# Optimization experiments

Hardware: AMD Instinct MI355X
Metric: run time of the kernel (lower is better)

## Reference

```python
import jax, jax.numpy as jnp
import numpy as np

T, B, H, W = 4, 8, 480, 640
N = 4_000_000


def setup_inputs() -> dict:
    key = jax.random.key(0)
    k1, k2, k3, k4 = jax.random.split(key, 4)
    # sorted batch ids (events grouped per sample)
    batch = jnp.sort(jax.random.randint(k1, (N,), 0, B)).astype(jnp.int32)
    # x,y normalized to [0,1]; t sorted globally => sorted within each batch
    xy = jax.random.uniform(k2, (N, 2), dtype=jnp.float32)
    t = jnp.sort(jax.random.uniform(k3, (N,), dtype=jnp.float32))
    pos = jnp.concatenate([xy, t[:, None]], axis=1)  # [N,3]
    feat = jax.random.normal(k4, (N, 1), dtype=jnp.float32)  # polarity = feat[:,0] > 0
    return {"pos": pos, "feat": feat, "batch": batch}


def _voxelize(pos, feat, batch):
    n = pos.shape[0]
    bids = jnp.arange(B, dtype=batch.dtype)
    left = jnp.searchsorted(batch, bids, side="left")
    right = jnporig = jnp.searchsorted(batch, bids, side="right")
    first = jnp.clip(left, 0, n - 1)
    last = jnp.clip(right - 1, 0, n - 1)

    t = pos[:, 2]
    cnt = right - left
    # torch: if t[-1] == t[0] (and >=2 events), bump last event's t by 1
    bump = ((cnt >= 2) & (t[last] == t[first])).astype(t.dtype)
    t = t.at[last].add(bump)

    t0b = t[first]                       # per-batch t[0]
    denom = t[last] - t0b                # per-batch t[-1]-t[0]
    denom = jnp.where(denom == 0, 1.0, denom)  # guard degenerate segments
    tn = (T - 1) * (t - t0b[batch]) / denom[batch]  # [N]

    xf = pos[:, 0] * (W - 1)
    yf = pos[:, 1] * (H - 1)
    x0 = xf.astype(jnp.int32)
    y0 = yf.astype(jnp.int32)
    t0 = tn.astype(jnp.int32)
    ch = jnp.where(feat[:, 0] > 0, 0, 1).astype(jnp.int32)  # pos->chan0, neg->chan1

    # 8 trilinear corners: offsets in {0,1}^3, shape [8,1] broadcast vs [N]
    offs = jnp.array([[dx, dy, dt] for dx in (0, 1) for dy in (0, 1) for dt in (0, 1)], dtype=jnp.int32)
    xl = x0[None, :] + offs[:, 0:1]  # [8,N]
    yl = y0[None, :] + offs[:, 1:2]
    tl = t0[None, :] + offs[:, 2:3]

    m = (xl >= 0) & (xl < W) & (yl >= 0) & (yl < H) & (tl >= 0) & (tl < T)
    w = (1 - jnp.abs(xl - xf[None, :])) * (1 - jnp.abs(yl - yf[None, :])) * (1 - jnp.abs(tl - tn[None, :]))

    bb = batch[None, :].astype(jnp.int32)
    idx = (((tl * B + bb) * 2 + ch[None, :]) * H + yl) * W + xl  # flat into [T,B,2,H,W]
    idx = jnp.where(m, idx, 0)
    w = jnp.where(m, w, 0.0)

    out = jnp.zeros(T * B * 2 * H * W, dtype=jnp.float32).at[idx.ravel()].add(w.ravel())
    return out.reshape(T, B, 2, H, W)


def reference(pos, feat, batch) -> jnp.ndarray:
    return _voxelize(pos, feat, batch)
```

## Files before the change

### kernel.cpp

```cpp
#include <hip/hip_runtime.h>

#define TT 4
#define BB 8
#define HH 480
#define WW 640
#define YSTR 4
#define NYB (HH/YSTR)
#define NBINS2 (BB*TT*NYB)
#define CAP2 2048
#define PPB2 1536
#define FTH 512
#define ITER (PPB2/FTH)
#define SBINS 1024
#define STAGECAP 2112
#define RROWS 4
#define NSTRIPE (HH/RROWS)
#define GTH 512
#define SPILL 0x80000000u
#define FXSCALE 524288.0f
#define FXINV (1.0f/524288.0f)

struct BatchParams { float t0b; float denom; int last; int bump; };

__global__ void setup_kernel(const float* __restrict__ pos, const int* __restrict__ batch,
                             int n, BatchParams* __restrict__ bp, int* __restrict__ rights) {
    int b = threadIdx.x;
    if (b >= BB) return;
    int lo = 0, hi = n;
    while (lo < hi) { int mid = (lo + hi) >> 1; if (batch[mid] < b) lo = mid + 1; else hi = mid; }
    int left = lo;
    lo = left; hi = n;
    while (lo < hi) { int mid = (lo + hi) >> 1; if (batch[mid] <= b) lo = mid + 1; else hi = mid; }
    int right = lo;
    int first = min(max(left, 0), n - 1);
    int last  = min(max(right - 1, 0), n - 1);
    int cnt   = right - left;
    float tf = pos[(size_t)first * 3 + 2];
    float tl = pos[(size_t)last  * 3 + 2];
    int bump = (cnt >= 2 && tl == tf) ? 1 : 0;
    float d = (tl + (float)bump) - tf;
    if (d == 0.0f) d = 1.0f;
    bp[b].t0b = tf; bp[b].denom = d; bp[b].last = last; bp[b].bump = bump;
    rights[b] = right;
}

__device__ __forceinline__ int b_of(const int* __restrict__ sr, int i) {
    int b = 0;
    #pragma unroll
    for (int w = 0; w < BB; ++w) b += (i >= sr[w]) ? 1 : 0;
    return b;
}

__global__ __launch_bounds__(FTH) void fill6_kernel(
        const float* __restrict__ pos, const float* __restrict__ feat,
        const BatchParams* __restrict__ bp, const int* __restrict__ rights,
        unsigned int* __restrict__ cursor, uint2* __restrict__ binidx, int n) {
    __shared__ uint2 stage[STAGECAP];
    __shared__ unsigned int addrbuf[STAGECAP];
    __shared__ unsigned int hist[SBINS];
    __shared__ int          dlt[SBINS];
    __shared__ unsigned int wavesum[8];
    __shared__ unsigned int totloc;
    __shared__ BatchParams sbp[BB];
    __shared__ int sr[BB];
    int tid = threadIdx.x;
    if (tid < BB) { sbp[tid] = bp[tid]; sr[tid] = rights[tid]; }
    hist[2 * tid] = 0; hist[2 * tid + 1] = 0;
    __syncthreads();

    int lo = blockIdx.x * PPB2;

    float px[ITER], py[ITER], ptv[ITER], fv[ITER];
    #pragma unroll
    for (int it = 0; it < ITER; ++it) {
        int i = lo + it * FTH + tid;
        if (i < n) {
            px[it]  = pos[(size_t)i * 3 + 0];
            py[it]  = pos[(size_t)i * 3 + 1];
            ptv[it] = pos[(size_t)i * 3 + 2];
            fv[it]  = feat[i];
        }
    }
    {
        int b0 = b_of(sr, lo);
        BatchParams p0 = sbp[b0];
        float t0v = pos[(size_t)lo * 3 + 2];
        if (p0.bump && lo == p0.last) t0v += 1.0f;
        float tn0 = (float)(TT - 1) * (t0v - p0.t0b) / p0.denom;
        int g_lo = b0 * TT + (int)tn0;
        wavesum[0] = (unsigned int)(g_lo * NYB);
    }
    __syncthreads();
    int binbase_lo = (int)wavesum[0];
    __syncthreads();

    unsigned int rx[ITER], ry[ITER], pm[ITER], ph[ITER];
    int keyv[ITER], hkeyv[ITER];
    #pragma unroll
    for (int it = 0; it < ITER; ++it) {
        int i = lo + it * FTH + tid;
        keyv[it] = -1; hkeyv[it] = -1;
        if (i < n) {
            int b = b_of(sr, i);
            BatchParams p = sbp[b];
            float t = ptv[it];
            if (p.bump && i == p.last) t += 1.0f;
            float tn = (float)(TT - 1) * (t - p.t0b) / p.denom;
            float xf = px[it] * (float)(WW - 1);
            float yf = py[it] * (float)(HH - 1);
            int x0 = (int)xf, y0 = (int)yf, t0 = (int)tn;
            float fx = xf - (float)x0;
            float fy = yf - (float)y0;
            float ft = tn - (float)t0;
            unsigned int ch = (fv[it] > 0.0f) ? 0u : 1u;
            unsigned int rin = (unsigned int)(y0 & 3);
            rx[it] = (unsigned int)x0 | (ch << 10) | (rin << 11)
                   | (((unsigned int)(fx * 4095.0f + 0.5f)) << 20);
            ry[it] = ((unsigned int)(fy * 65535.0f + 0.5f))
                   | (((unsigned int)(ft * 65535.0f + 0.5f)) << 16);
            int g = b * TT + t0;
            int key = g * NYB + (y0 >> 2);
            keyv[it] = key;
            int lb = key - binbase_lo;
            pm[it] = ((unsigned)lb < SBINS) ? atomicAdd(&hist[lb], 1u) : SPILL;
            if (rin == 3u && (y0 >> 2) < NYB - 1) {
                hkeyv[it] = key + 1;
                int lbh = lb + 1;
                ph[it] = ((unsigned)lbh < SBINS) ? atomicAdd(&hist[lbh], 1u) : SPILL;
            }
        }
    }
    __syncthreads();
    unsigned int c0 = hist[2 * tid], c1 = hist[2 * tid + 1];
    unsigned int sum = c0 + c1;
    int lane = tid & 63, wid = tid >> 6;
    unsigned int scan = sum;
    #pragma unroll
    for (int off = 1; off < 64; off <<= 1) {
        unsigned int v = __shfl_up(scan, off, 64);
        if (lane >= off) scan += v;
    }
    if (lane == 63) wavesum[wid] = scan;
    __syncthreads();
    unsigned int woff = 0;
    #pragma unroll
    for (int w = 0; w < 8; ++w) woff += (w < wid) ? wavesum[w] : 0u;
    unsigned int incl = woff + scan;
    unsigned int base = incl - sum;
    if (tid == FTH - 1) totloc = incl;
    {
        unsigned int lp0 = base, lp1 = base + c0;
        int bin0 = binbase_lo + 2 * tid;
        unsigned int gb0 = 0, gb1 = 0;
        if (c0 && (unsigned)bin0     < NBINS2) gb0 = atomicAdd(&cursor[bin0],     c0);
        if (c1 && (unsigned)(bin0+1) < NBINS2) gb1 = atomicAdd(&cursor[bin0 + 1], c1);
        dlt[2 * tid]     = (int)gb0 - (int)lp0;
        dlt[2 * tid + 1] = (int)gb1 - (int)lp1;
        hist[2 * tid] = lp0; hist[2 * tid + 1] = lp1;
    }
    __syncthreads();
    #pragma unroll
    for (int it = 0; it < ITER; ++it) {
        if (keyv[it] < 0) continue;
        #pragma unroll
        for (int h = 0; h < 2; ++h) {
            int key = h ? hkeyv[it] : keyv[it];
            if (key < 0) continue;
            unsigned int p = h ? ph[it] : pm[it];
            uint2 rec; rec.x = h ? (rx[it] | (1u << 13)) : rx[it]; rec.y = ry[it];
            if (p & SPILL) {
                unsigned int slot = atomicAdd(&cursor[key], 1u);
                if (slot < CAP2) binidx[(size_t)key * CAP2 + slot] = rec;
            } else {
                int lb = key - binbase_lo;
                unsigned int sl = hist[lb] + p;
                unsigned int off = (unsigned int)(dlt[lb] + (int)sl);
                if (sl < STAGECAP) {
                    stage[sl] = rec;
                    addrbuf[sl] = (off < CAP2) ? (unsigned int)key * CAP2 + off
                                               : 0xFFFFFFFFu;
                } else if (off < CAP2) {
                    binidx[(size_t)key * CAP2 + off] = rec;
                }
            }
        }
    }
    __syncthreads();
    unsigned int tot = min(totloc, (unsigned int)STAGECAP);
    for (unsigned int k = tid; k < tot; k += FTH) {
        unsigned int a = addrbuf[k];
        if (a != 0xFFFFFFFFu) binidx[a] = stage[k];
    }
}

__device__ __forceinline__ void gather_rec(unsigned long long* tile, uint2 rec, int q) {
    int x0   = (int)(rec.x & 1023u);
    int ch   = (int)((rec.x >> 10) & 1u);
    int rin  = (int)((rec.x >> 11) & 3u);
    int halo = (int)((rec.x >> 13) & 1u);
    float fx = (float)((rec.x >> 20) & 4095u) * (1.0f / 4095.0f);
    float fy = (float)(rec.y & 65535u) * (1.0f / 65535.0f);
    float ft = (float)(rec.y >> 16) * (1.0f / 65535.0f);
    float wt = q ? (1.0f - ft) : ft;
    float w1 = wt * fy;
    unsigned long long p1 =
          (unsigned long long)(unsigned int)fmaf(w1 * (1.0f - fx), FXSCALE, 0.5f)
        | ((unsigned long long)(unsigned int)fmaf(w1 * fx, FXSCALE, 0.5f) << 32);
    if (halo) {
        atomicAdd(&tile[(ch * RROWS) * WW + x0], p1);
    } else {
        float w0 = wt * (1.0f - fy);
        unsigned long long p0 =
              (unsigned long long)(unsigned int)fmaf(w0 * (1.0f - fx), FXSCALE, 0.5f)
            | ((unsigned long long)(unsigned int)fmaf(w0 * fx, FXSCALE, 0.5f) << 32);
        unsigned long long* rowp = &tile[(ch * RROWS + rin) * WW + x0];
        atomicAdd(rowp, p0);
        if (rin < RROWS - 1) atomicAdd(rowp + WW, p1);
    }
}

__global__ __launch_bounds__(GTH) void gather7_kernel(
        const unsigned int* __restrict__ cursor, const uint2* __restrict__ binidx,
        float* __restrict__ out) {
    __shared__ unsigned long long tile[2 * RROWS * WW];
    __shared__ unsigned int cnt[2];
    int bid = blockIdx.x;
    int s  = bid % NSTRIPE;
    int bt = bid / NSTRIPE;
    int tl = bt % TT;
    int b  = bt / TT;
    int r0 = s * RROWS;
    int tid = threadIdx.x;

    if (tid < 2) {
        int t0r = tl - 1 + tid;
        unsigned int c = 0;
        if (t0r >= 0) c = min(cursor[(b * TT + t0r) * NYB + s], (unsigned int)CAP2);
        cnt[tid] = c;
    }
    for (int k = tid; k < 2 * RROWS * WW; k += GTH) tile[k] = 0ull;
    __syncthreads();

    #pragma unroll
    for (int q = 0; q < 2; ++q) {
        int t0r = tl - 1 + q;
        if (t0r < 0) continue;
        unsigned int base = (unsigned int)((b * TT + t0r) * NYB + s) * CAP2;
        unsigned int c = cnt[q];
        unsigned int m = tid;
        if (m < c) {
            uint2 rec = binidx[base + m];
            for (;;) {
                unsigned int m2 = m + GTH;
                bool has2 = m2 < c;
                uint2 rec2;
                if (has2) rec2 = binidx[base + m2];
                gather_rec(tile, rec, q);
                if (!has2) break;
                rec = rec2; m = m2;
            }
        }
    }
    __syncthreads();
    const unsigned int* t32 = (const unsigned int*)tile;
    const int QUADS = 2 * RROWS * WW / 4;
    for (int qd = tid; qd < QUADS; qd += GTH) {
        int e = qd * 4;
        uint4 A = *(const uint4*)&t32[e * 2];
        uint4 B = *(const uint4*)&t32[e * 2 + 4];
        unsigned int cc = (e % WW == 0) ? 0u : t32[e * 2 - 1];
        float4 v;
        v.x = (float)(A.x + cc)  * FXINV;
        v.y = (float)(A.z + A.y) * FXINV;
        v.z = (float)(B.x + A.w) * FXINV;
        v.w = (float)(B.z + B.y) * FXINV;
        int ch  = e / (RROWS * WW);
        int rem = e % (RROWS * WW);
        int r   = rem / WW;
        int x   = rem % WW;
        *(float4*)&out[((((size_t)tl * BB + b) * 2 + ch) * HH + (r0 + r)) * WW + x] = v;
    }
}

__global__ void voxel_kernel(const float* __restrict__ pos, const float* __restrict__ feat,
                             const int* __restrict__ batch, const BatchParams* __restrict__ bp,
                             float* __restrict__ out, int n) {
    __shared__ BatchParams sbp[BB];
    if (threadIdx.x < BB) sbp[threadIdx.x] = bp[threadIdx.x];
    __syncthreads();
    int i = blockIdx.x * blockDim.x + threadIdx.x;
    if (i >= n) return;
    int b = batch[i];
    float x = pos[(size_t)i * 3 + 0];
    float y = pos[(size_t)i * 3 + 1];
    float t = pos[(size_t)i * 3 + 2];
    BatchParams p = sbp[b];
    if (p.bump && i == p.last) t += 1.0f;
    float tn = (float)(TT - 1) * (t - p.t0b) / p.denom;
    float xf = x * (float)(WW - 1);
    float yf = y * (float)(HH - 1);
    int x0 = (int)xf, y0 = (int)yf, t0 = (int)tn;
    float fx = xf - (float)x0, fy = yf - (float)y0, ft = tn - (float)t0;
    int ch = (feat[i] > 0.0f) ? 0 : 1;
    float wx[2] = {1.0f - fx, fx};
    float wy[2] = {1.0f - fy, fy};
    float wt[2] = {1.0f - ft, ft};
    #pragma unroll
    for (int dt = 0; dt < 2; ++dt) {
        int tlc = t0 + dt;
        if (tlc < 0 || tlc >= TT) continue;
        #pragma unroll
        for (int dy = 0; dy < 2; ++dy) {
            int yl = y0 + dy;
            if (yl < 0 || yl >= HH) continue;
            #pragma unroll
            for (int dx = 0; dx < 2; ++dx) {
                int xl = x0 + dx;
                if (xl < 0 || xl >= WW) continue;
                float w = wx[dx] * wy[dy] * wt[dt];
                size_t idx = ((((size_t)tlc * BB + b) * 2 + ch) * (size_t)HH + yl) * (size_t)WW + xl;
                atomicAdd(&out[idx], w);
            }
        }
    }
}

extern "C" void kernel_launch(void* const* d_in, const int* in_sizes, int n_in,
                              void* d_out, int out_size, void* d_ws, size_t ws_size,
                              hipStream_t stream) {
    const float* pos   = (const float*)d_in[0];
    const float* feat  = (const float*)d_in[1];
    const int*   batch = (const int*)d_in[2];
    float* out = (float*)d_out;
    int n = in_sizes[2];

    char* ws = (char*)d_ws;
    BatchParams* bp      = (BatchParams*)ws;
    int*          rights = (int*)(ws + 512);
    unsigned int* cursor = (unsigned int*)(ws + 1024);
    uint2*        binidx = (uint2*)(ws + 65536);
    size_t need = 65536 + (size_t)NBINS2 * CAP2 * sizeof(uint2);

    if (ws_size >= need) {
        hipMemsetAsync(cursor, 0, NBINS2 * sizeof(unsigned int), stream);
        setup_kernel<<<1, 64, 0, stream>>>(pos, batch, n, bp, rights);
        int nblocks = (n + PPB2 - 1) / PPB2;
        fill6_kernel<<<nblocks, FTH, 0, stream>>>(pos, feat, bp, rights, cursor, binidx, n);
        gather7_kernel<<<BB * TT * NSTRIPE, GTH, 0, stream>>>(cursor, binidx, out);
    } else {
        hipMemsetAsync(d_out, 0, (size_t)out_size * sizeof(float), stream);
        setup_kernel<<<1, 64, 0, stream>>>(pos, batch, n, bp, rights);
        int blocks = (n + 255) / 256;
        voxel_kernel<<<blocks, 256, 0, stream>>>(pos, feat, batch, bp, out, n);
    }
}
```

Before: 91.93 us.

## Split stripe bins into main and halo sub-bins instead of duplicating halo records

Events whose y falls in the last row of a 4-row stripe are no longer written twice, once to their own bin and once as a halo copy to the next stripe. Each stripe now has two sub-bins: a main bin (cap 1280) and a row-3 bin (cap 512). The gather kernel reads the main bin, its own row-3 bin and the previous stripe's row-3 bin, then applies the matching row weights. This removes the duplicate writes and shrinks both the workspace and the staging buffer. The trade-off is fixed per-bin capacities that could drop events if a sub-bin overflows, and removed staging-overflow guards that assume the staging buffer always fits.

```diff
diff --git a/kernel.cpp b/kernel.cpp
--- a/kernel.cpp
+++ b/kernel.cpp
@@ -6,13 +6,16 @@
 #define WW 640
 #define YSTR 4
 #define NYB (HH/YSTR)
-#define NBINS2 (BB*TT*NYB)
-#define CAP2 2048
+#define NSTRIPES (BB*TT*NYB)
+#define CAPA 1280
+#define CAPB 512
+#define STRCAP (CAPA+CAPB)
+#define NKEYS (NSTRIPES*2)
 #define PPB2 1536
 #define FTH 512
 #define ITER (PPB2/FTH)
 #define SBINS 1024
-#define STAGECAP 2112
+#define STAGECAP 1536
 #define RROWS 4
 #define NSTRIPE (HH/RROWS)
 #define GTH 512
@@ -51,7 +54,7 @@
     return b;
 }
 
-__global__ __launch_bounds__(FTH) void fill6_kernel(
+__global__ __launch_bounds__(FTH) void fill7_kernel(
         const float* __restrict__ pos, const float* __restrict__ feat,
         const BatchParams* __restrict__ bp, const int* __restrict__ rights,
         unsigned int* __restrict__ cursor, uint2* __restrict__ binidx, int n) {
@@ -61,6 +64,7 @@
     __shared__ int          dlt[SBINS];
     __shared__ unsigned int wavesum[8];
     __shared__ unsigned int totloc;
+    __shared__ int sh_binbase;
     __shared__ BatchParams sbp[BB];
     __shared__ int sr[BB];
     int tid = threadIdx.x;
@@ -81,25 +85,24 @@
             fv[it]  = feat[i];
         }
     }
-    {
+    if (tid == 0) {
         int b0 = b_of(sr, lo);
         BatchParams p0 = sbp[b0];
-        float t0v = pos[(size_t)lo * 3 + 2];
+        float t0v = ptv[0];
         if (p0.bump && lo == p0.last) t0v += 1.0f;
         float tn0 = (float)(TT - 1) * (t0v - p0.t0b) / p0.denom;
         int g_lo = b0 * TT + (int)tn0;
-        wavesum[0] = (unsigned int)(g_lo * NYB);
-    }
-    __syncthreads();
-    int binbase_lo = (int)wavesum[0];
-    __syncthreads();
-
-    unsigned int rx[ITER], ry[ITER], pm[ITER], ph[ITER];
-    int keyv[ITER], hkeyv[ITER];
+        sh_binbase = g_lo * NYB * 2;
+    }
+    __syncthreads();
+    int binbase_lo = sh_binbase;
+
+    unsigned int rx[ITER], ry[ITER], pm[ITER];
+    int keyv[ITER];
     #pragma unroll
     for (int it = 0; it < ITER; ++it) {
         int i = lo + it * FTH + tid;
-        keyv[it] = -1; hkeyv[it] = -1;
+        keyv[it] = -1;
         if (i < n) {
             int b = b_of(sr, i);
             BatchParams p = sbp[b];
@@ -119,15 +122,11 @@
             ry[it] = ((unsigned int)(fy * 65535.0f + 0.5f))
                    | (((unsigned int)(ft * 65535.0f + 0.5f)) << 16);
             int g = b * TT + t0;
-            int key = g * NYB + (y0 >> 2);
-            keyv[it] = key;
-            int lb = key - binbase_lo;
+            int stripe = g * NYB + (y0 >> 2);
+            int key2 = stripe * 2 + (rin == 3u ? 1 : 0);
+            keyv[it] = key2;
+            int lb = key2 - binbase_lo;
             pm[it] = ((unsigned)lb < SBINS) ? atomicAdd(&hist[lb], 1u) : SPILL;
-            if (rin == 3u && (y0 >> 2) < NYB - 1) {
-                hkeyv[it] = key + 1;
-                int lbh = lb + 1;
-                ph[it] = ((unsigned)lbh < SBINS) ? atomicAdd(&hist[lbh], 1u) : SPILL;
-            }
         }
     }
     __syncthreads();
@@ -152,8 +151,8 @@
         unsigned int lp0 = base, lp1 = base + c0;
         int bin0 = binbase_lo + 2 * tid;
         unsigned int gb0 = 0, gb1 = 0;
-        if (c0 && (unsigned)bin0     < NBINS2) gb0 = atomicAdd(&cursor[bin0],     c0);
-        if (c1 && (unsigned)(bin0+1) < NBINS2) gb1 = atomicAdd(&cursor[bin0 + 1], c1);
+        if (c0 && (unsigned)bin0       < NKEYS) gb0 = atomicAdd(&cursor[bin0],     c0);
+        if (c1 && (unsigned)(bin0 + 1) < NKEYS) gb1 = atomicAdd(&cursor[bin0 + 1], c1);
         dlt[2 * tid]     = (int)gb0 - (int)lp0;
         dlt[2 * tid + 1] = (int)gb1 - (int)lp1;
         hist[2 * tid] = lp0; hist[2 * tid + 1] = lp1;
@@ -161,28 +160,21 @@
     __syncthreads();
     #pragma unroll
     for (int it = 0; it < ITER; ++it) {
-        if (keyv[it] < 0) continue;
-        #pragma unroll
-        for (int h = 0; h < 2; ++h) {
-            int key = h ? hkeyv[it] : keyv[it];
-            if (key < 0) continue;
-            unsigned int p = h ? ph[it] : pm[it];
-            uint2 rec; rec.x = h ? (rx[it] | (1u << 13)) : rx[it]; rec.y = ry[it];
-            if (p & SPILL) {
-                unsigned int slot = atomicAdd(&cursor[key], 1u);
-                if (slot < CAP2) binidx[(size_t)key * CAP2 + slot] = rec;
-            } else {
-                int lb = key - binbase_lo;
-                unsigned int sl = hist[lb] + p;
-                unsigned int off = (unsigned int)(dlt[lb] + (int)sl);
-                if (sl < STAGECAP) {
-                    stage[sl] = rec;
-                    addrbuf[sl] = (off < CAP2) ? (unsigned int)key * CAP2 + off
-                                               : 0xFFFFFFFFu;
-                } else if (off < CAP2) {
-                    binidx[(size_t)key * CAP2 + off] = rec;
-                }
-            }
+        int key2 = keyv[it];
+        if (key2 < 0) continue;
+        unsigned int p = pm[it];
+        unsigned int cap  = (key2 & 1) ? CAPB : CAPA;
+        unsigned int rbase = (unsigned int)(key2 >> 1) * STRCAP + ((key2 & 1) ? CAPA : 0u);
+        uint2 rec; rec.x = rx[it]; rec.y = ry[it];
+        if (p & SPILL) {
+            unsigned int slot = atomicAdd(&cursor[key2], 1u);
+            if (slot < cap) binidx[(size_t)rbase + slot] = rec;
+        } else {
+            int lb = key2 - binbase_lo;
+            unsigned int sl  = hist[lb] + p;
+            unsigned int off = (unsigned int)(dlt[lb] + (int)sl);
+            stage[sl] = rec;
+            addrbuf[sl] = (off < cap) ? rbase + off : 0xFFFFFFFFu;
         }
     }
     __syncthreads();
@@ -193,37 +185,29 @@
     }
 }
 
-__device__ __forceinline__ void gather_rec(unsigned long long* tile, uint2 rec, int q) {
-    int x0   = (int)(rec.x & 1023u);
-    int ch   = (int)((rec.x >> 10) & 1u);
-    int rin  = (int)((rec.x >> 11) & 3u);
-    int halo = (int)((rec.x >> 13) & 1u);
-    float fx = (float)((rec.x >> 20) & 4095u) * (1.0f / 4095.0f);
+__device__ __forceinline__ void dec_w(uint2 rec, int q, int* x0, int* ch, int* rin,
+                                      float* w0, float* w1) {
+    *x0  = (int)(rec.x & 1023u);
+    *ch  = (int)((rec.x >> 10) & 1u);
+    *rin = (int)((rec.x >> 11) & 3u);
     float fy = (float)(rec.y & 65535u) * (1.0f / 65535.0f);
     float ft = (float)(rec.y >> 16) * (1.0f / 65535.0f);
     float wt = q ? (1.0f - ft) : ft;
-    float w1 = wt * fy;
-    unsigned long long p1 =
-          (unsigned long long)(unsigned int)fmaf(w1 * (1.0f - fx), FXSCALE, 0.5f)
-        | ((unsigned long long)(unsigned int)fmaf(w1 * fx, FXSCALE, 0.5f) << 32);
-    if (halo) {
-        atomicAdd(&tile[(ch * RROWS) * WW + x0], p1);
-    } else {
-        float w0 = wt * (1.0f - fy);
-        unsigned long long p0 =
-              (unsigned long long)(unsigned int)fmaf(w0 * (1.0f - fx), FXSCALE, 0.5f)
-            | ((unsigned long long)(unsigned int)fmaf(w0 * fx, FXSCALE, 0.5f) << 32);
-        unsigned long long* rowp = &tile[(ch * RROWS + rin) * WW + x0];
-        atomicAdd(rowp, p0);
-        if (rin < RROWS - 1) atomicAdd(rowp + WW, p1);
-    }
-}
-
-__global__ __launch_bounds__(GTH) void gather7_kernel(
+    *w0 = wt * (1.0f - fy);
+    *w1 = wt * fy;
+}
+__device__ __forceinline__ unsigned long long packw(uint2 rec, float w) {
+    float fx = (float)((rec.x >> 20) & 4095u) * (1.0f / 4095.0f);
+    return (unsigned long long)(unsigned int)fmaf(w * (1.0f - fx), FXSCALE, 0.5f)
+         | ((unsigned long long)(unsigned int)fmaf(w * fx, FXSCALE, 0.5f) << 32);
+}
+
+__global__ __launch_bounds__(GTH) void gather8_kernel(
         const unsigned int* __restrict__ cursor, const uint2* __restrict__ binidx,
         float* __restrict__ out) {
     __shared__ unsigned long long tile[2 * RROWS * WW];
-    __shared__ unsigned int cnt[2];
+    __shared__ unsigned int cnt[6];
+    __shared__ unsigned int sbase[6];
     int bid = blockIdx.x;
     int s  = bid % NSTRIPE;
     int bt = bid / NSTRIPE;
@@ -232,32 +216,73 @@
     int r0 = s * RROWS;
     int tid = threadIdx.x;
 
-    if (tid < 2) {
-        int t0r = tl - 1 + tid;
-        unsigned int c = 0;
-        if (t0r >= 0) c = min(cursor[(b * TT + t0r) * NYB + s], (unsigned int)CAP2);
-        cnt[tid] = c;
+    if (tid < 6) {
+        int q = tid / 3, ty = tid % 3;
+        int t0r = tl - 1 + q;
+        unsigned int c = 0, ba = 0;
+        if (t0r >= 0 && (ty != 2 || s > 0)) {
+            int sp = (ty == 2) ? s - 1 : s;
+            int stripe = (b * TT + t0r) * NYB + sp;
+            int isB = (ty != 0);
+            c  = min(cursor[stripe * 2 + isB], isB ? (unsigned)CAPB : (unsigned)CAPA);
+            ba = (unsigned int)stripe * STRCAP + (isB ? CAPA : 0u);
+        }
+        cnt[tid] = c; sbase[tid] = ba;
     }
     for (int k = tid; k < 2 * RROWS * WW; k += GTH) tile[k] = 0ull;
     __syncthreads();
 
     #pragma unroll
     for (int q = 0; q < 2; ++q) {
-        int t0r = tl - 1 + q;
-        if (t0r < 0) continue;
-        unsigned int base = (unsigned int)((b * TT + t0r) * NYB + s) * CAP2;
-        unsigned int c = cnt[q];
-        unsigned int m = tid;
-        if (m < c) {
-            uint2 rec = binidx[base + m];
-            for (;;) {
-                unsigned int m2 = m + GTH;
-                bool has2 = m2 < c;
-                uint2 rec2;
-                if (has2) rec2 = binidx[base + m2];
-                gather_rec(tile, rec, q);
-                if (!has2) break;
-                rec = rec2; m = m2;
+        if (tl - 1 + q < 0) continue;
+        {
+            unsigned int base = sbase[q * 3 + 0], c = cnt[q * 3 + 0];
+            unsigned int m = tid;
+            if (m < c) {
+                uint2 rec = binidx[base + m];
+                for (;;) {
+                    unsigned int m2 = m + GTH; bool has2 = m2 < c;
+                    uint2 rec2; if (has2) rec2 = binidx[base + m2];
+                    int x0, ch, rin; float w0, w1;
+                    dec_w(rec, q, &x0, &ch, &rin, &w0, &w1);
+                    unsigned long long* rowp = &tile[(ch * RROWS + rin) * WW + x0];
+                    atomicAdd(rowp, packw(rec, w0));
+                    atomicAdd(rowp + WW, packw(rec, w1));
+                    if (!has2) break;
+                    rec = rec2; m = m2;
+                }
+            }
+        }
+        {
+            unsigned int base = sbase[q * 3 + 1], c = cnt[q * 3 + 1];
+            unsigned int m = tid;
+            if (m < c) {
+                uint2 rec = binidx[base + m];
+                for (;;) {
+                    unsigned int m2 = m + GTH; bool has2 = m2 < c;
+                    uint2 rec2; if (has2) rec2 = binidx[base + m2];
+                    int x0, ch, rin; float w0, w1;
+                    dec_w(rec, q, &x0, &ch, &rin, &w0, &w1);
+                    atomicAdd(&tile[(ch * RROWS + 3) * WW + x0], packw(rec, w0));
+                    if (!has2) break;
+                    rec = rec2; m = m2;
+                }
+            }
+        }
+        {
+            unsigned int base = sbase[q * 3 + 2], c = cnt[q * 3 + 2];
+            unsigned int m = tid;
+            if (m < c) {
+                uint2 rec = binidx[base + m];
+                for (;;) {
+                    unsigned int m2 = m + GTH; bool has2 = m2 < c;
+                    uint2 rec2; if (has2) rec2 = binidx[base + m2];
+                    int x0, ch, rin; float w0, w1;
+                    dec_w(rec, q, &x0, &ch, &rin, &w0, &w1);
+                    atomicAdd(&tile[(ch * RROWS + 0) * WW + x0], packw(rec, w1));
+                    if (!has2) break;
+                    rec = rec2; m = m2;
+                }
             }
         }
     }
@@ -339,14 +364,14 @@
     int*          rights = (int*)(ws + 512);
     unsigned int* cursor = (unsigned int*)(ws + 1024);
     uint2*        binidx = (uint2*)(ws + 65536);
-    size_t need = 65536 + (size_t)NBINS2 * CAP2 * sizeof(uint2);
+    size_t need = 65536 + (size_t)NSTRIPES * STRCAP * sizeof(uint2);
 
     if (ws_size >= need) {
-        hipMemsetAsync(cursor, 0, NBINS2 * sizeof(unsigned int), stream);
+        hipMemsetAsync(cursor, 0, NKEYS * sizeof(unsigned int), stream);
         setup_kernel<<<1, 64, 0, stream>>>(pos, batch, n, bp, rights);
         int nblocks = (n + PPB2 - 1) / PPB2;
-        fill6_kernel<<<nblocks, FTH, 0, stream>>>(pos, feat, bp, rights, cursor, binidx, n);
-        gather7_kernel<<<BB * TT * NSTRIPE, GTH, 0, stream>>>(cursor, binidx, out);
+        fill7_kernel<<<nblocks, FTH, 0, stream>>>(pos, feat, bp, rights, cursor, binidx, n);
+        gather8_kernel<<<BB * TT * NSTRIPE, GTH, 0, stream>>>(cursor, binidx, out);
     } else {
         hipMemsetAsync(d_out, 0, (size_t)out_size * sizeof(float), stream);
         setup_kernel<<<1, 64, 0, stream>>>(pos, batch, n, bp, rights);
```

Result: faster. 89.57 us (-2.6%).
